# Kernel optimization log

Measured on AMD Instinct MI355X. Metric: run time of the kernel, lower is better.

Reference implementation:

```python
import jax, jax.numpy as jnp
import numpy as np

HIDDEN = 64
INPUT_DIM = 128
DEMO_DIM = 12
ATT_WIDTH = 1e7  # history_only=True, attention_width=None -> causal


def setup_inputs() -> dict:
    key = jax.random.key(0)
    ks = jax.random.split(key, 8)
    B, T = 4, 512
    inp = {
        "input": jax.random.normal(ks[0], (B, T, INPUT_DIM), dtype=jnp.float32),
        "demo": jax.random.normal(ks[1], (B, DEMO_DIM), dtype=jnp.float32),
        "Wt": jax.random.normal(ks[2], (INPUT_DIM, HIDDEN), dtype=jnp.float32) * 0.08,
        "Wx": jax.random.normal(ks[3], (INPUT_DIM, HIDDEN), dtype=jnp.float32) * 0.08,
        "Wd": jax.random.normal(ks[4], (DEMO_DIM, HIDDEN), dtype=jnp.float32) * 0.25,
        "bh": jnp.zeros((HIDDEN,), dtype=jnp.float32),
        "Wa": jax.random.normal(ks[5], (HIDDEN, 1), dtype=jnp.float32) * 0.12,
        "ba": jnp.zeros((1,), dtype=jnp.float32),
    }
    return inp


def reference(input, demo, Wt, Wx, Wd, bh, Wa, ba):
    B, T, D = input.shape
    # additive attention scores via broadcasted [B,T,T,H] intermediate
    q = (input @ Wt)[:, :, None, :]          # [B,T,1,H]
    k = (input @ Wx)[:, None, :, :]          # [B,1,T,H]
    d = (demo @ Wd)[:, None, None, :]        # [B,1,1,H]
    h = jnp.tanh(q + k + d + bh)             # [B,T,T,H]
    e = (h @ Wa)[..., 0] + ba[0]             # [B,T,T]
    # custom softmax: exp(e - rowmax) BEFORE masking, then mask, then normalize
    e = jnp.exp(e - jnp.max(e, axis=-1, keepdims=True))
    idx = jnp.arange(T, dtype=jnp.float32)
    lower = idx[:, None] - (ATT_WIDTH - 1.0)  # history_only
    upper = lower + ATT_WIDTH
    mask = ((lower <= idx[None, :]) & (idx[None, :] < upper)).astype(e.dtype)
    e = e * mask
    s = jnp.sum(e, axis=-1, keepdims=True)
    e = e / (s + 1e-7)
    v = jnp.einsum('bts,bsd->btd', e, input)  # [B,T,D]
    return (v, e)
```

## Files before the change

kernel.cpp:

```cpp
#include <hip/hip_runtime.h>
#include <math.h>

#define B_ 4
#define T_ 512
#define D_ 128
#define H_ 64
#define DEMO_ 12
#define LOG2E 1.4426950408889634f
#define SC2   (2.0f * LOG2E)

typedef float float2v __attribute__((ext_vector_type(2)));

__global__ __launch_bounds__(256) void prep_kernel(
    const float* __restrict__ input, const float* __restrict__ demo,
    const float* __restrict__ Wt, const float* __restrict__ Wx,
    const float* __restrict__ Wd, const float* __restrict__ bh,
    const float* __restrict__ Wa, const float* __restrict__ ba,
    float* __restrict__ Q, float* __restrict__ K2T, float* __restrict__ Cs)
{
    __shared__ float in_sh[8 * D_];
    int tid  = threadIdx.x;
    int row0 = blockIdx.x * 8;
    int b    = row0 >> 9;

    #pragma unroll
    for (int k = 0; k < 4; ++k)
        in_sh[tid + 256 * k] = input[row0 * D_ + tid + 256 * k];
    __syncthreads();

    int h  = tid & 63;
    int rr = tid >> 6;

    float dB = bh[h];
    #pragma unroll
    for (int kk = 0; kk < DEMO_; ++kk)
        dB = fmaf(demo[b * DEMO_ + kk], Wd[kk * H_ + h], dB);

    float q0 = 0.f, q1 = 0.f, x0 = 0.f, x1 = 0.f;
    #pragma unroll 8
    for (int k = 0; k < D_; ++k) {
        float wt = Wt[k * H_ + h];
        float wx = Wx[k * H_ + h];
        float a0 = in_sh[rr * D_ + k];
        float a1 = in_sh[(rr + 4) * D_ + k];
        q0 = fmaf(a0, wt, q0);
        q1 = fmaf(a1, wt, q1);
        x0 = fmaf(a0, wx, x0);
        x1 = fmaf(a1, wx, x1);
    }

    int ra = row0 + rr, rb = row0 + rr + 4;
    Q[ra * H_ + h] = q0 * SC2;
    Q[rb * H_ + h] = q1 * SC2;
    int ta = ra & (T_ - 1), tb = rb & (T_ - 1);
    K2T[(b * H_ + h) * T_ + ta] = (x0 + dB) * SC2;
    K2T[(b * H_ + h) * T_ + tb] = (x1 + dB) * SC2;

    if (blockIdx.x == 0 && tid < 64) {
        float w = Wa[tid];
        #pragma unroll
        for (int off = 32; off; off >>= 1) w += __shfl_down(w, off, 64);
        if (tid == 0) Cs[0] = (ba[0] + w) * LOG2E;
    }
}

__global__ __launch_bounds__(512, 8) void attn_kernel(
    const float* __restrict__ input,
    const float* __restrict__ Qs, const float* __restrict__ K2T,
    const float* __restrict__ Wa, const float* __restrict__ Cs,
    float* __restrict__ out_v, float* __restrict__ out_e)
{
    __shared__ float p_sh[T_ * 2];
    __shared__ float red_m[8 * 2];
    __shared__ float red_s[8 * 2];
    __shared__ float partial[4][2 * D_];

    int tid  = threadIdx.x;
    int bx   = blockIdx.x;
    int b    = blockIdx.y;
    int y    = ((bx & 7) << 5) | (bx >> 3);
    int i0   = 2 * y, i1 = i0 + 1;
    int lane = tid & 63, wv = tid >> 6;
    int j    = tid;

    const float* qr0 = Qs + (size_t)(b * T_ + i0) * H_;
    const float* qr1 = qr0 + H_;
    const float* k2p = K2T + (size_t)b * H_ * T_ + j;
    float CL = Cs[0];

    float eg0 = -INFINITY, eg1 = -INFINITY;
    if ((wv << 6) <= i1) {
        float acc0 = 0.f, acc1 = 0.f;
        #pragma unroll 2
        for (int h0 = 0; h0 < H_; h0 += 8) {
            float kv[8];
            #pragma unroll
            for (int u = 0; u < 8; ++u)
                kv[u] = k2p[(size_t)(h0 + u) * T_];
            #pragma unroll
            for (int u = 0; u < 8; ++u) {
                float wa = Wa[h0 + u];
                float q0 = qr0[h0 + u], q1 = qr1[h0 + u];
                float ex0 = __builtin_amdgcn_exp2f(q0 + kv[u]);
                float ex1 = __builtin_amdgcn_exp2f(q1 + kv[u]);
                acc0 = fmaf(wa, __builtin_amdgcn_rcpf(1.0f + ex0), acc0);
                acc1 = fmaf(wa, __builtin_amdgcn_rcpf(1.0f + ex1), acc1);
            }
        }
        if (j <= i0) eg0 = fmaf(-2.0f * LOG2E, acc0, CL);
        if (j <= i1) eg1 = fmaf(-2.0f * LOG2E, acc1, CL);
    }

    float M0 = eg0, M1 = eg1;
    #pragma unroll
    for (int off = 32; off; off >>= 1) {
        M0 = fmaxf(M0, __shfl_down(M0, off, 64));
        M1 = fmaxf(M1, __shfl_down(M1, off, 64));
    }
    if (lane == 0) ((float2v*)red_m)[wv] = (float2v){M0, M1};
    __syncthreads();
    {
        float2v m = ((float2v*)red_m)[0];
        #pragma unroll
        for (int w = 1; w < 8; ++w) {
            float2v mw = ((float2v*)red_m)[w];
            m[0] = fmaxf(m[0], mw[0]);
            m[1] = fmaxf(m[1], mw[1]);
        }
        M0 = m[0]; M1 = m[1];
    }

    float p0 = (j <= i0) ? __builtin_amdgcn_exp2f(eg0 - M0) : 0.0f;
    float p1 = (j <= i1) ? __builtin_amdgcn_exp2f(eg1 - M1) : 0.0f;
    *(float2v*)&p_sh[j * 2] = (float2v){p0, p1};
    float S0 = p0, S1 = p1;
    #pragma unroll
    for (int off = 32; off; off >>= 1) {
        S0 += __shfl_down(S0, off, 64);
        S1 += __shfl_down(S1, off, 64);
    }
    if (lane == 0) ((float2v*)red_s)[wv] = (float2v){S0, S1};
    __syncthreads();

    float inv0, inv1;
    {
        float2v s = ((float2v*)red_s)[0];
        #pragma unroll
        for (int w = 1; w < 8; ++w) {
            float2v sw = ((float2v*)red_s)[w];
            s[0] += sw[0]; s[1] += sw[1];
        }
        inv0 = __builtin_amdgcn_rcpf(s[0] + 1e-7f);
        inv1 = __builtin_amdgcn_rcpf(s[1] + 1e-7f);
    }

    out_e[((size_t)(b * T_ + i0)) * T_ + j] = p0 * inv0;
    out_e[((size_t)(b * T_ + i1)) * T_ + j] = p1 * inv1;

    {
        int d  = tid & 127;
        int s4 = tid >> 7;
        float va0 = 0.f, va1 = 0.f;
        if ((s4 << 7) <= i1) {
            const float* inp = input + ((size_t)(b * T_) + (s4 << 7)) * D_ + d;
            const float* pp  = p_sh + (s4 << 7) * 2;
            #pragma unroll 4
            for (int jj = 0; jj < 128; ++jj) {
                float x = inp[(size_t)jj * D_];
                float2v p2 = *(const float2v*)&pp[jj * 2];
                va0 = fmaf(p2[0], x, va0);
                va1 = fmaf(p2[1], x, va1);
            }
        }
        partial[s4][d]      = va0;
        partial[s4][D_ + d] = va1;
    }
    __syncthreads();

    if (tid < 256) {
        int r  = tid >> 7;
        int dd = tid & 127;
        float v = partial[0][r * D_ + dd] + partial[1][r * D_ + dd]
                + partial[2][r * D_ + dd] + partial[3][r * D_ + dd];
        float inv = r ? inv1 : inv0;
        out_v[(size_t)(b * T_ + i0 + r) * D_ + dd] = v * inv;
    }
}

extern "C" void kernel_launch(void* const* d_in, const int* in_sizes, int n_in,
                              void* d_out, int out_size, void* d_ws, size_t ws_size,
                              hipStream_t stream)
{
    const float* input = (const float*)d_in[0];
    const float* demo  = (const float*)d_in[1];
    const float* Wt    = (const float*)d_in[2];
    const float* Wx    = (const float*)d_in[3];
    const float* Wd    = (const float*)d_in[4];
    const float* bh    = (const float*)d_in[5];
    const float* Wa    = (const float*)d_in[6];
    const float* ba    = (const float*)d_in[7];

    float* out_v = (float*)d_out;
    float* out_e = out_v + (size_t)B_ * T_ * D_;

    float* Q   = (float*)d_ws;
    float* K2T = Q + (size_t)B_ * T_ * H_;
    float* Cs  = K2T + (size_t)B_ * H_ * T_;

    prep_kernel<<<dim3(B_ * T_ / 8), 256, 0, stream>>>(input, demo, Wt, Wx, Wd, bh,
                                                       Wa, ba, Q, K2T, Cs);
    attn_kernel<<<dim3(256, B_), 512, 0, stream>>>(input, Q, K2T, Wa, Cs, out_v, out_e);
}
```

Before: 100.5 us.

## Pair short and long causal rows per block to balance attention work

Each attention block now handles four query rows: two early rows and their mirror rows from the end of the sequence. This evens out the triangular causal workload across blocks and lets each loaded K value feed four exp/rcp chains. Query vectors are staged in shared memory, and the PV accumulation is rewritten with float4 loads over 16 row slices. The grid halves to 128 blocks per batch, occupancy hints drop, and the larger shared partial buffer may reduce resident blocks.

```diff
diff --git a/kernel.cpp b/kernel.cpp
--- a/kernel.cpp
+++ b/kernel.cpp
@@ -9,6 +9,7 @@
 #define LOG2E 1.4426950408889634f
 #define SC2   (2.0f * LOG2E)
 
+typedef float float4v __attribute__((ext_vector_type(4)));
 typedef float float2v __attribute__((ext_vector_type(2)));
 
 __global__ __launch_bounds__(256) void prep_kernel(
@@ -64,127 +65,171 @@
     }
 }
 
-__global__ __launch_bounds__(512, 8) void attn_kernel(
+__global__ __launch_bounds__(512, 4) void attn_kernel(
     const float* __restrict__ input,
     const float* __restrict__ Qs, const float* __restrict__ K2T,
     const float* __restrict__ Wa, const float* __restrict__ Cs,
     float* __restrict__ out_v, float* __restrict__ out_e)
 {
-    __shared__ float p_sh[T_ * 2];
-    __shared__ float red_m[8 * 2];
-    __shared__ float red_s[8 * 2];
-    __shared__ float partial[4][2 * D_];
+    __shared__ float   qsh[H_ * 4];
+    __shared__ float   p_sh[T_ * 4];
+    __shared__ float4v red_m[8];
+    __shared__ float4v red_s[8];
+    __shared__ float   partial[16][4 * D_];
 
     int tid  = threadIdx.x;
-    int bx   = blockIdx.x;
+    int y    = blockIdx.x;
     int b    = blockIdx.y;
-    int y    = ((bx & 7) << 5) | (bx >> 3);
-    int i0   = 2 * y, i1 = i0 + 1;
     int lane = tid & 63, wv = tid >> 6;
     int j    = tid;
-
-    const float* qr0 = Qs + (size_t)(b * T_ + i0) * H_;
-    const float* qr1 = qr0 + H_;
+    int iA0  = 2 * y,       iA1 = iA0 + 1;
+    int iB0  = 510 - 2 * y, iB1 = iB0 + 1;
+
+    if (tid < 256) {
+        int h  = tid >> 2, r = tid & 3;
+        int ir = (r < 2) ? (iA0 + r) : (iB0 + r - 2);
+        qsh[tid] = Qs[(size_t)(b * T_ + ir) * H_ + h];
+    }
+    __syncthreads();
+
     const float* k2p = K2T + (size_t)b * H_ * T_ + j;
-    float CL = Cs[0];
-
-    float eg0 = -INFINITY, eg1 = -INFINITY;
-    if ((wv << 6) <= i1) {
-        float acc0 = 0.f, acc1 = 0.f;
+    float CL   = Cs[0];
+    bool  actA = (wv << 6) <= iA1;
+    bool  actB = (wv << 6) <= iB1;
+
+    float aA0 = 0.f, aA1 = 0.f, aB0 = 0.f, aB1 = 0.f;
+    if (actA) {
         #pragma unroll 2
         for (int h0 = 0; h0 < H_; h0 += 8) {
             float kv[8];
             #pragma unroll
-            for (int u = 0; u < 8; ++u)
-                kv[u] = k2p[(size_t)(h0 + u) * T_];
+            for (int u = 0; u < 8; ++u) kv[u] = k2p[(size_t)(h0 + u) * T_];
             #pragma unroll
             for (int u = 0; u < 8; ++u) {
-                float wa = Wa[h0 + u];
-                float q0 = qr0[h0 + u], q1 = qr1[h0 + u];
-                float ex0 = __builtin_amdgcn_exp2f(q0 + kv[u]);
-                float ex1 = __builtin_amdgcn_exp2f(q1 + kv[u]);
-                acc0 = fmaf(wa, __builtin_amdgcn_rcpf(1.0f + ex0), acc0);
-                acc1 = fmaf(wa, __builtin_amdgcn_rcpf(1.0f + ex1), acc1);
+                float wa   = Wa[h0 + u];
+                float4v q4 = *(const float4v*)&qsh[(h0 + u) * 4];
+                float e0 = __builtin_amdgcn_exp2f(q4[0] + kv[u]);
+                float e1 = __builtin_amdgcn_exp2f(q4[1] + kv[u]);
+                float e2 = __builtin_amdgcn_exp2f(q4[2] + kv[u]);
+                float e3 = __builtin_amdgcn_exp2f(q4[3] + kv[u]);
+                aA0 = fmaf(wa, __builtin_amdgcn_rcpf(1.0f + e0), aA0);
+                aA1 = fmaf(wa, __builtin_amdgcn_rcpf(1.0f + e1), aA1);
+                aB0 = fmaf(wa, __builtin_amdgcn_rcpf(1.0f + e2), aB0);
+                aB1 = fmaf(wa, __builtin_amdgcn_rcpf(1.0f + e3), aB1);
             }
         }
-        if (j <= i0) eg0 = fmaf(-2.0f * LOG2E, acc0, CL);
-        if (j <= i1) eg1 = fmaf(-2.0f * LOG2E, acc1, CL);
-    }
-
-    float M0 = eg0, M1 = eg1;
+    } else if (actB) {
+        #pragma unroll 2
+        for (int h0 = 0; h0 < H_; h0 += 8) {
+            float kv[8];
+            #pragma unroll
+            for (int u = 0; u < 8; ++u) kv[u] = k2p[(size_t)(h0 + u) * T_];
+            #pragma unroll
+            for (int u = 0; u < 8; ++u) {
+                float wa   = Wa[h0 + u];
+                float2v q2 = *(const float2v*)&qsh[(h0 + u) * 4 + 2];
+                float e2 = __builtin_amdgcn_exp2f(q2[0] + kv[u]);
+                float e3 = __builtin_amdgcn_exp2f(q2[1] + kv[u]);
+                aB0 = fmaf(wa, __builtin_amdgcn_rcpf(1.0f + e2), aB0);
+                aB1 = fmaf(wa, __builtin_amdgcn_rcpf(1.0f + e3), aB1);
+            }
+        }
+    }
+
+    float eg0 = (j <= iA0) ? fmaf(-SC2, aA0, CL) : -INFINITY;
+    float eg1 = (j <= iA1) ? fmaf(-SC2, aA1, CL) : -INFINITY;
+    float eg2 = (j <= iB0) ? fmaf(-SC2, aB0, CL) : -INFINITY;
+    float eg3 = (j <= iB1) ? fmaf(-SC2, aB1, CL) : -INFINITY;
+
+    float M0 = eg0, M1 = eg1, M2 = eg2, M3 = eg3;
     #pragma unroll
     for (int off = 32; off; off >>= 1) {
         M0 = fmaxf(M0, __shfl_down(M0, off, 64));
         M1 = fmaxf(M1, __shfl_down(M1, off, 64));
-    }
-    if (lane == 0) ((float2v*)red_m)[wv] = (float2v){M0, M1};
-    __syncthreads();
-    {
-        float2v m = ((float2v*)red_m)[0];
+        M2 = fmaxf(M2, __shfl_down(M2, off, 64));
+        M3 = fmaxf(M3, __shfl_down(M3, off, 64));
+    }
+    if (lane == 0) red_m[wv] = (float4v){M0, M1, M2, M3};
+    __syncthreads();
+    {
+        float4v m = red_m[0];
         #pragma unroll
         for (int w = 1; w < 8; ++w) {
-            float2v mw = ((float2v*)red_m)[w];
-            m[0] = fmaxf(m[0], mw[0]);
-            m[1] = fmaxf(m[1], mw[1]);
-        }
-        M0 = m[0]; M1 = m[1];
-    }
-
-    float p0 = (j <= i0) ? __builtin_amdgcn_exp2f(eg0 - M0) : 0.0f;
-    float p1 = (j <= i1) ? __builtin_amdgcn_exp2f(eg1 - M1) : 0.0f;
-    *(float2v*)&p_sh[j * 2] = (float2v){p0, p1};
-    float S0 = p0, S1 = p1;
+            float4v mw = red_m[w];
+            m[0] = fmaxf(m[0], mw[0]); m[1] = fmaxf(m[1], mw[1]);
+            m[2] = fmaxf(m[2], mw[2]); m[3] = fmaxf(m[3], mw[3]);
+        }
+        M0 = m[0]; M1 = m[1]; M2 = m[2]; M3 = m[3];
+    }
+
+    float p0 = (j <= iA0) ? __builtin_amdgcn_exp2f(eg0 - M0) : 0.0f;
+    float p1 = (j <= iA1) ? __builtin_amdgcn_exp2f(eg1 - M1) : 0.0f;
+    float p2 = (j <= iB0) ? __builtin_amdgcn_exp2f(eg2 - M2) : 0.0f;
+    float p3 = (j <= iB1) ? __builtin_amdgcn_exp2f(eg3 - M3) : 0.0f;
+    *(float4v*)&p_sh[j * 4] = (float4v){p0, p1, p2, p3};
+
+    float S0 = p0, S1 = p1, S2 = p2, S3 = p3;
     #pragma unroll
     for (int off = 32; off; off >>= 1) {
         S0 += __shfl_down(S0, off, 64);
         S1 += __shfl_down(S1, off, 64);
-    }
-    if (lane == 0) ((float2v*)red_s)[wv] = (float2v){S0, S1};
-    __syncthreads();
-
-    float inv0, inv1;
-    {
-        float2v s = ((float2v*)red_s)[0];
+        S2 += __shfl_down(S2, off, 64);
+        S3 += __shfl_down(S3, off, 64);
+    }
+    if (lane == 0) red_s[wv] = (float4v){S0, S1, S2, S3};
+    __syncthreads();
+
+    float inv0, inv1, inv2, inv3;
+    {
+        float4v s = red_s[0];
         #pragma unroll
         for (int w = 1; w < 8; ++w) {
-            float2v sw = ((float2v*)red_s)[w];
-            s[0] += sw[0]; s[1] += sw[1];
+            float4v sw = red_s[w];
+            s[0] += sw[0]; s[1] += sw[1]; s[2] += sw[2]; s[3] += sw[3];
         }
         inv0 = __builtin_amdgcn_rcpf(s[0] + 1e-7f);
         inv1 = __builtin_amdgcn_rcpf(s[1] + 1e-7f);
-    }
-
-    out_e[((size_t)(b * T_ + i0)) * T_ + j] = p0 * inv0;
-    out_e[((size_t)(b * T_ + i1)) * T_ + j] = p1 * inv1;
-
-    {
-        int d  = tid & 127;
-        int s4 = tid >> 7;
-        float va0 = 0.f, va1 = 0.f;
-        if ((s4 << 7) <= i1) {
-            const float* inp = input + ((size_t)(b * T_) + (s4 << 7)) * D_ + d;
-            const float* pp  = p_sh + (s4 << 7) * 2;
+        inv2 = __builtin_amdgcn_rcpf(s[2] + 1e-7f);
+        inv3 = __builtin_amdgcn_rcpf(s[3] + 1e-7f);
+    }
+
+    {
+        int s  = tid >> 5, d4 = tid & 31;
+        float4v va0 = {0,0,0,0}, va1 = {0,0,0,0}, va2 = {0,0,0,0}, va3 = {0,0,0,0};
+        if ((s << 5) <= iB1) {
+            const float* inp = input + ((size_t)(b * T_) + (s << 5)) * D_ + (d4 << 2);
+            const float* pp  = p_sh + (s << 5) * 4;
             #pragma unroll 4
-            for (int jj = 0; jj < 128; ++jj) {
-                float x = inp[(size_t)jj * D_];
-                float2v p2 = *(const float2v*)&pp[jj * 2];
-                va0 = fmaf(p2[0], x, va0);
-                va1 = fmaf(p2[1], x, va1);
+            for (int jj = 0; jj < 32; ++jj) {
+                float4v x  = *(const float4v*)(inp + (size_t)jj * D_);
+                float4v p4 = *(const float4v*)(pp + jj * 4);
+                va0 += x * p4[0];
+                va1 += x * p4[1];
+                va2 += x * p4[2];
+                va3 += x * p4[3];
             }
         }
-        partial[s4][d]      = va0;
-        partial[s4][D_ + d] = va1;
-    }
-    __syncthreads();
-
-    if (tid < 256) {
-        int r  = tid >> 7;
-        int dd = tid & 127;
-        float v = partial[0][r * D_ + dd] + partial[1][r * D_ + dd]
-                + partial[2][r * D_ + dd] + partial[3][r * D_ + dd];
-        float inv = r ? inv1 : inv0;
-        out_v[(size_t)(b * T_ + i0 + r) * D_ + dd] = v * inv;
-    }
+        *(float4v*)&partial[s][0 * D_ + (d4 << 2)] = va0;
+        *(float4v*)&partial[s][1 * D_ + (d4 << 2)] = va1;
+        *(float4v*)&partial[s][2 * D_ + (d4 << 2)] = va2;
+        *(float4v*)&partial[s][3 * D_ + (d4 << 2)] = va3;
+    }
+    __syncthreads();
+
+    {
+        int r  = tid >> 7, d = tid & 127;
+        float v = 0.f;
+        #pragma unroll
+        for (int ss = 0; ss < 16; ++ss) v += partial[ss][r * D_ + d];
+        int   ir  = (r < 2) ? (iA0 + r) : (iB0 + r - 2);
+        float inv = (r == 0) ? inv0 : (r == 1) ? inv1 : (r == 2) ? inv2 : inv3;
+        out_v[(size_t)(b * T_ + ir) * D_ + d] = v * inv;
+    }
+
+    out_e[((size_t)(b * T_ + iA0)) * T_ + j] = p0 * inv0;
+    out_e[((size_t)(b * T_ + iA1)) * T_ + j] = p1 * inv1;
+    out_e[((size_t)(b * T_ + iB0)) * T_ + j] = p2 * inv2;
+    out_e[((size_t)(b * T_ + iB1)) * T_ + j] = p3 * inv3;
 }
 
 extern "C" void kernel_launch(void* const* d_in, const int* in_sizes, int n_in,
@@ -209,5 +254,5 @@
 
     prep_kernel<<<dim3(B_ * T_ / 8), 256, 0, stream>>>(input, demo, Wt, Wx, Wd, bh,
                                                        Wa, ba, Q, K2T, Cs);
-    attn_kernel<<<dim3(256, B_), 512, 0, stream>>>(input, Q, K2T, Wa, Cs, out_v, out_e);
+    attn_kernel<<<dim3(128, B_), 512, 0, stream>>>(input, Q, K2T, Wa, Cs, out_v, out_e);
 }
```

Result: faster. 92.71 us (-7.7%).

## Pair mirrored causal rows per block to balance work and vectorize PV

Applied to the files above, without the earlier changes.

Each 1024-thread block now handles four query rows: the pair 2y,2y+1 together with the mirrored pair 510-2y,511-2y. This balances the triangular causal workload across blocks and halves the grid. Q rows are staged in shared memory, and the probability-times-input product is reorganized into 32 row slices using float4 loads with four accumulators, followed by a 32-way shared reduction. The trade-offs are larger shared memory (a 64KB partial buffer), lower occupancy, and a heavier final reduction.

```diff
diff --git a/kernel.cpp b/kernel.cpp
--- a/kernel.cpp
+++ b/kernel.cpp
@@ -9,6 +9,7 @@
 #define LOG2E 1.4426950408889634f
 #define SC2   (2.0f * LOG2E)
 
+typedef float float4v __attribute__((ext_vector_type(4)));
 typedef float float2v __attribute__((ext_vector_type(2)));
 
 __global__ __launch_bounds__(256) void prep_kernel(
@@ -64,52 +65,60 @@
     }
 }
 
-__global__ __launch_bounds__(512, 8) void attn_kernel(
+__global__ __launch_bounds__(1024, 8) void attn_kernel(
     const float* __restrict__ input,
     const float* __restrict__ Qs, const float* __restrict__ K2T,
     const float* __restrict__ Wa, const float* __restrict__ Cs,
     float* __restrict__ out_v, float* __restrict__ out_e)
 {
-    __shared__ float p_sh[T_ * 2];
-    __shared__ float red_m[8 * 2];
-    __shared__ float red_s[8 * 2];
-    __shared__ float partial[4][2 * D_];
+    __shared__ float   qsh[H_ * 4];
+    __shared__ float   p_sh[T_ * 4];
+    __shared__ float2v red_m[16];
+    __shared__ float2v red_s[16];
+    __shared__ float   partial[32][4 * D_];
 
     int tid  = threadIdx.x;
-    int bx   = blockIdx.x;
+    int y    = blockIdx.x;
     int b    = blockIdx.y;
-    int y    = ((bx & 7) << 5) | (bx >> 3);
-    int i0   = 2 * y, i1 = i0 + 1;
     int lane = tid & 63, wv = tid >> 6;
-    int j    = tid;
-
-    const float* qr0 = Qs + (size_t)(b * T_ + i0) * H_;
-    const float* qr1 = qr0 + H_;
+    int j    = tid & (T_ - 1);
+    int u    = tid >> 9;
+    int iA0  = 2 * y,       iA1 = iA0 + 1;
+    int iB0  = 510 - 2 * y, iB1 = iB0 + 1;
+    int i0u  = u ? iB0 : iA0;
+    int i1u  = i0u + 1;
+
+    if (tid < 256) {
+        int h  = tid >> 2, r = tid & 3;
+        int ir = (r < 2) ? (iA0 + r) : (iB0 + r - 2);
+        qsh[tid] = Qs[(size_t)(b * T_ + ir) * H_ + h];
+    }
+    __syncthreads();
+
     const float* k2p = K2T + (size_t)b * H_ * T_ + j;
     float CL = Cs[0];
 
-    float eg0 = -INFINITY, eg1 = -INFINITY;
-    if ((wv << 6) <= i1) {
-        float acc0 = 0.f, acc1 = 0.f;
+    float a0 = 0.f, a1 = 0.f;
+    if ((j & ~63) <= i1u) {
         #pragma unroll 2
         for (int h0 = 0; h0 < H_; h0 += 8) {
             float kv[8];
             #pragma unroll
-            for (int u = 0; u < 8; ++u)
-                kv[u] = k2p[(size_t)(h0 + u) * T_];
+            for (int uu = 0; uu < 8; ++uu) kv[uu] = k2p[(size_t)(h0 + uu) * T_];
             #pragma unroll
-            for (int u = 0; u < 8; ++u) {
-                float wa = Wa[h0 + u];
-                float q0 = qr0[h0 + u], q1 = qr1[h0 + u];
-                float ex0 = __builtin_amdgcn_exp2f(q0 + kv[u]);
-                float ex1 = __builtin_amdgcn_exp2f(q1 + kv[u]);
-                acc0 = fmaf(wa, __builtin_amdgcn_rcpf(1.0f + ex0), acc0);
-                acc1 = fmaf(wa, __builtin_amdgcn_rcpf(1.0f + ex1), acc1);
+            for (int uu = 0; uu < 8; ++uu) {
+                float wa   = Wa[h0 + uu];
+                float2v q2 = *(const float2v*)&qsh[(h0 + uu) * 4 + 2 * u];
+                float e0 = __builtin_amdgcn_exp2f(q2[0] + kv[uu]);
+                float e1 = __builtin_amdgcn_exp2f(q2[1] + kv[uu]);
+                a0 = fmaf(wa, __builtin_amdgcn_rcpf(1.0f + e0), a0);
+                a1 = fmaf(wa, __builtin_amdgcn_rcpf(1.0f + e1), a1);
             }
         }
-        if (j <= i0) eg0 = fmaf(-2.0f * LOG2E, acc0, CL);
-        if (j <= i1) eg1 = fmaf(-2.0f * LOG2E, acc1, CL);
-    }
+    }
+
+    float eg0 = (j <= i0u) ? fmaf(-SC2, a0, CL) : -INFINITY;
+    float eg1 = (j <= i1u) ? fmaf(-SC2, a1, CL) : -INFINITY;
 
     float M0 = eg0, M1 = eg1;
     #pragma unroll
@@ -117,73 +126,80 @@
         M0 = fmaxf(M0, __shfl_down(M0, off, 64));
         M1 = fmaxf(M1, __shfl_down(M1, off, 64));
     }
-    if (lane == 0) ((float2v*)red_m)[wv] = (float2v){M0, M1};
+    if (lane == 0) red_m[wv] = (float2v){M0, M1};
     __syncthreads();
     {
-        float2v m = ((float2v*)red_m)[0];
+        float2v m = red_m[u * 8];
         #pragma unroll
         for (int w = 1; w < 8; ++w) {
-            float2v mw = ((float2v*)red_m)[w];
+            float2v mw = red_m[u * 8 + w];
             m[0] = fmaxf(m[0], mw[0]);
             m[1] = fmaxf(m[1], mw[1]);
         }
         M0 = m[0]; M1 = m[1];
     }
 
-    float p0 = (j <= i0) ? __builtin_amdgcn_exp2f(eg0 - M0) : 0.0f;
-    float p1 = (j <= i1) ? __builtin_amdgcn_exp2f(eg1 - M1) : 0.0f;
-    *(float2v*)&p_sh[j * 2] = (float2v){p0, p1};
+    float p0 = (j <= i0u) ? __builtin_amdgcn_exp2f(eg0 - M0) : 0.0f;
+    float p1 = (j <= i1u) ? __builtin_amdgcn_exp2f(eg1 - M1) : 0.0f;
+    *(float2v*)&p_sh[j * 4 + 2 * u] = (float2v){p0, p1};
+
     float S0 = p0, S1 = p1;
     #pragma unroll
     for (int off = 32; off; off >>= 1) {
         S0 += __shfl_down(S0, off, 64);
         S1 += __shfl_down(S1, off, 64);
     }
-    if (lane == 0) ((float2v*)red_s)[wv] = (float2v){S0, S1};
-    __syncthreads();
-
-    float inv0, inv1;
+    if (lane == 0) red_s[wv] = (float2v){S0, S1};
+    __syncthreads();
+
+    float inv[4];
     {
-        float2v s = ((float2v*)red_s)[0];
+        float2v sA = red_s[0], sB = red_s[8];
         #pragma unroll
         for (int w = 1; w < 8; ++w) {
-            float2v sw = ((float2v*)red_s)[w];
-            s[0] += sw[0]; s[1] += sw[1];
-        }
-        inv0 = __builtin_amdgcn_rcpf(s[0] + 1e-7f);
-        inv1 = __builtin_amdgcn_rcpf(s[1] + 1e-7f);
-    }
-
-    out_e[((size_t)(b * T_ + i0)) * T_ + j] = p0 * inv0;
-    out_e[((size_t)(b * T_ + i1)) * T_ + j] = p1 * inv1;
+            float2v aw = red_s[w], bw = red_s[8 + w];
+            sA[0] += aw[0]; sA[1] += aw[1];
+            sB[0] += bw[0]; sB[1] += bw[1];
+        }
+        inv[0] = __builtin_amdgcn_rcpf(sA[0] + 1e-7f);
+        inv[1] = __builtin_amdgcn_rcpf(sA[1] + 1e-7f);
+        inv[2] = __builtin_amdgcn_rcpf(sB[0] + 1e-7f);
+        inv[3] = __builtin_amdgcn_rcpf(sB[1] + 1e-7f);
+    }
+
+    out_e[((size_t)(b * T_ + i0u)) * T_ + j] = p0 * inv[2 * u];
+    out_e[((size_t)(b * T_ + i1u)) * T_ + j] = p1 * inv[2 * u + 1];
 
     {
-        int d  = tid & 127;
-        int s4 = tid >> 7;
-        float va0 = 0.f, va1 = 0.f;
-        if ((s4 << 7) <= i1) {
-            const float* inp = input + ((size_t)(b * T_) + (s4 << 7)) * D_ + d;
-            const float* pp  = p_sh + (s4 << 7) * 2;
+        int s = tid >> 5, d4 = tid & 31;
+        float4v va0 = {0,0,0,0}, va1 = {0,0,0,0}, va2 = {0,0,0,0}, va3 = {0,0,0,0};
+        if ((s << 4) <= iB1) {
+            const float* inp = input + ((size_t)(b * T_) + (s << 4)) * D_ + (d4 << 2);
+            const float* pp  = p_sh + (s << 4) * 4;
             #pragma unroll 4
-            for (int jj = 0; jj < 128; ++jj) {
-                float x = inp[(size_t)jj * D_];
-                float2v p2 = *(const float2v*)&pp[jj * 2];
-                va0 = fmaf(p2[0], x, va0);
-                va1 = fmaf(p2[1], x, va1);
+            for (int jj = 0; jj < 16; ++jj) {
+                float4v x  = *(const float4v*)(inp + (size_t)jj * D_);
+                float4v p4 = *(const float4v*)(pp + jj * 4);
+                va0 += x * p4[0];
+                va1 += x * p4[1];
+                va2 += x * p4[2];
+                va3 += x * p4[3];
             }
         }
-        partial[s4][d]      = va0;
-        partial[s4][D_ + d] = va1;
-    }
-    __syncthreads();
-
-    if (tid < 256) {
-        int r  = tid >> 7;
-        int dd = tid & 127;
-        float v = partial[0][r * D_ + dd] + partial[1][r * D_ + dd]
-                + partial[2][r * D_ + dd] + partial[3][r * D_ + dd];
-        float inv = r ? inv1 : inv0;
-        out_v[(size_t)(b * T_ + i0 + r) * D_ + dd] = v * inv;
+        *(float4v*)&partial[s][0 * D_ + (d4 << 2)] = va0;
+        *(float4v*)&partial[s][1 * D_ + (d4 << 2)] = va1;
+        *(float4v*)&partial[s][2 * D_ + (d4 << 2)] = va2;
+        *(float4v*)&partial[s][3 * D_ + (d4 << 2)] = va3;
+    }
+    __syncthreads();
+
+    if (tid < 512) {
+        int r = tid >> 7, d = tid & 127;
+        float v = 0.f;
+        #pragma unroll
+        for (int ss = 0; ss < 32; ++ss) v += partial[ss][r * D_ + d];
+        int ir = (r < 2) ? (iA0 + r) : (iB0 + r - 2);
+        out_v[(size_t)(b * T_ + ir) * D_ + d] = v * inv[r];
     }
 }
 
@@ -209,5 +225,5 @@
 
     prep_kernel<<<dim3(B_ * T_ / 8), 256, 0, stream>>>(input, demo, Wt, Wx, Wd, bh,
                                                        Wa, ba, Q, K2T, Cs);
-    attn_kernel<<<dim3(256, B_), 512, 0, stream>>>(input, Q, K2T, Wa, Cs, out_v, out_e);
+    attn_kernel<<<dim3(128, B_), 1024, 0, stream>>>(input, Q, K2T, Wa, Cs, out_v, out_e);
 }
```

Result: faster. 93.18 us (-7.3%).
